# Optimization experiments

Hardware: AMD Instinct MI355X
Metric: run time of the kernel (lower is better)

The kernel has to match this reference:

```python
import jax, jax.numpy as jnp
import numpy as np


def setup_inputs() -> dict:
    key = jax.random.key(0)
    k1, k2, k3, k4 = jax.random.split(key, 4)
    B, T, L, C, F = 1024, 128, 256, 2, 784
    x = jax.random.normal(k1, (B, T, F), dtype=jnp.float32)
    W = jax.random.normal(k2, (L, F), dtype=jnp.float32) * (1.0 / np.sqrt(F))
    b = jax.random.normal(k3, (L,), dtype=jnp.float32) * 0.01
    contribution = jax.random.normal(k4, (T, L, C), dtype=jnp.float32)
    return {"x": x, "W": W, "b": b, "contribution": contribution}


def reference(x, W, b, contribution):
    # symbolic_paths: Linear(784 -> leaf) + Hardtanh  -> [B, T, L]
    sp = jnp.clip(jnp.einsum('btf,lf->btl', x, W) + b, -1.0, 1.0)
    # per-(tree,leaf) outer product: class_value[b,t,l,c] = sp[b,t,l] * contribution[t,l,c]
    cv = sp[..., None] * contribution[None]          # [B, T, L, C]
    p = jax.nn.softmax(cv, axis=-1)                  # softmax over classes
    gini = jnp.sum(1.0 - p * p, axis=-1)             # [B, T, L]
    return (sp, gini)
```

## Files before the change

### kernel.cpp

```cpp
#include <hip/hip_runtime.h>
#include <hip/hip_bf16.h>

typedef __attribute__((ext_vector_type(8))) short bf16x8;
typedef __attribute__((ext_vector_type(4))) float f32x4;

#define B_SZ   1024
#define T_SZ   128
#define L_SZ   256
#define F_SZ   784
#define M_TOT  (B_SZ * T_SZ)
#define BK     32
#define KSTEPS 25
#define KCHUNKS 100
#define BROWS  32

#define WPRE_ELEMS (KSTEPS * 4 * L_SZ)
#define WPRE_BYTES (WPRE_ELEMS * 16)
#define CDIFF_ELEMS (T_SZ * L_SZ)
#define WS_NEED (WPRE_BYTES + CDIFF_ELEMS * 4)

__device__ __forceinline__ unsigned short f2bf(float f) {
    __hip_bfloat16 h = __float2bfloat16(f);
    return *reinterpret_cast<unsigned short*>(&h);
}

__global__ __launch_bounds__(256) void dn_prep(
    const float* __restrict__ W, const float* __restrict__ contrib,
    unsigned short* __restrict__ wpre, float* __restrict__ cdiff)
{
    const int gid = blockIdx.x * 256 + threadIdx.x;
    if (gid < WPRE_ELEMS) {
        const int leaf = gid & 255;
        const int kg   = (gid >> 8) & 3;
        const int ks   = gid >> 10;
        const int k0   = ks * BK + kg * 8;
        bf16x8 v;
        #pragma unroll
        for (int j = 0; j < 8; ++j) {
            const int k = k0 + j;
            const float f = (k < F_SZ) ? W[(size_t)leaf * F_SZ + k] : 0.f;
            v[j] = (short)f2bf(f);
        }
        *reinterpret_cast<bf16x8*>(wpre + (size_t)gid * 8) = v;
    } else {
        const int cid = gid - WPRE_ELEMS;
        if (cid < CDIFF_ELEMS)
            cdiff[cid] = contrib[(size_t)cid * 2] - contrib[(size_t)cid * 2 + 1];
    }
}

__global__ __launch_bounds__(512, 6) void dn_fused7(
    const float* __restrict__ x, const unsigned short* __restrict__ wpre,
    const float* __restrict__ bias, const float* __restrict__ cdiff,
    float* __restrict__ out)
{
    __shared__ __align__(16) unsigned char smem[KCHUNKS * BROWS * 16];
    bf16x8* As = reinterpret_cast<bf16x8*>(smem);
    typedef float OtRow[264];
    OtRow* Ot = reinterpret_cast<OtRow*>(smem);

    const int tid  = threadIdx.x;
    const int lane = tid & 63;
    const int wid  = tid >> 6;
    const int lr   = lane & 15;
    const int kseg = lane >> 4;

    const int rowBase = blockIdx.x * BROWS;
    const int colBase = wid * 32;

    #pragma unroll
    for (int it = 0; it < 7; ++it) {
        const int i = it * 512 + tid;
        if (i < BROWS * KCHUNKS) {
            const int row = i / KCHUNKS;
            const int kc  = i - row * KCHUNKS;
            bf16x8 v;
            if (kc < 98) {
                const float* p = x + (size_t)(rowBase + row) * F_SZ + kc * 8;
                const f32x4 lo = *reinterpret_cast<const f32x4*>(p);
                const f32x4 hi = *reinterpret_cast<const f32x4*>(p + 4);
                #pragma unroll
                for (int j = 0; j < 4; ++j) {
                    v[j]     = (short)f2bf(lo[j]);
                    v[4 + j] = (short)f2bf(hi[j]);
                }
            } else {
                #pragma unroll
                for (int j = 0; j < 8; ++j) v[j] = 0;
            }
            As[kc * BROWS + (row ^ (kc & 7))] = v;
        }
    }
    __syncthreads();

    const unsigned short* wpb = wpre + ((size_t)kseg * L_SZ + colBase + lr) * 8;

    f32x4 acc[2][2];
    #pragma unroll
    for (int mi = 0; mi < 2; ++mi)
        #pragma unroll
        for (int ni = 0; ni < 2; ++ni)
            acc[mi][ni] = (f32x4){0.f, 0.f, 0.f, 0.f};

    bf16x8 wcur[2], wnxt[2];
    wcur[0] = *reinterpret_cast<const bf16x8*>(wpb);
    wcur[1] = *reinterpret_cast<const bf16x8*>(wpb + 128);

    #pragma unroll
    for (int ks = 0; ks < KSTEPS; ++ks) {
        if (ks + 1 < KSTEPS) {
            wnxt[0] = *reinterpret_cast<const bf16x8*>(wpb + (size_t)(ks + 1) * 8192);
            wnxt[1] = *reinterpret_cast<const bf16x8*>(wpb + (size_t)(ks + 1) * 8192 + 128);
        }
        const int kcr = ks * 4 + kseg;
        const bf16x8 a0 = As[kcr * BROWS + (lr ^ (kcr & 7))];
        const bf16x8 a1 = As[kcr * BROWS + ((16 + lr) ^ (kcr & 7))];

        acc[0][0] = __builtin_amdgcn_mfma_f32_16x16x32_bf16(a0, wcur[0], acc[0][0], 0, 0, 0);
        acc[0][1] = __builtin_amdgcn_mfma_f32_16x16x32_bf16(a0, wcur[1], acc[0][1], 0, 0, 0);
        acc[1][0] = __builtin_amdgcn_mfma_f32_16x16x32_bf16(a1, wcur[0], acc[1][0], 0, 0, 0);
        acc[1][1] = __builtin_amdgcn_mfma_f32_16x16x32_bf16(a1, wcur[1], acc[1][1], 0, 0, 0);

        wcur[0] = wnxt[0];
        wcur[1] = wnxt[1];
    }
    __syncthreads();

    float spv[2][2][4];
    #pragma unroll
    for (int ni = 0; ni < 2; ++ni) {
        const float bb = bias[colBase + ni * 16 + lr];
        #pragma unroll
        for (int mi = 0; mi < 2; ++mi)
            #pragma unroll
            for (int r = 0; r < 4; ++r)
                spv[mi][ni][r] = fminf(fmaxf(acc[mi][ni][r] + bb, -1.f), 1.f);
    }

    const int erow = tid >> 4;
    const int ecol = (tid & 15) * 4;
    const size_t GOFF = (size_t)M_TOT * L_SZ;
    float* orow = out + (size_t)(rowBase + erow) * L_SZ;

    #pragma unroll
    for (int ni = 0; ni < 2; ++ni)
        #pragma unroll
        for (int mi = 0; mi < 2; ++mi)
            #pragma unroll
            for (int r = 0; r < 4; ++r)
                Ot[mi * 16 + kseg * 4 + r][colBase + ni * 16 + lr] = spv[mi][ni][r];
    __syncthreads();
    #pragma unroll
    for (int j = 0; j < 4; ++j) {
        const f32x4 v = *reinterpret_cast<const f32x4*>(&Ot[erow][ecol + 64 * j]);
        *reinterpret_cast<f32x4*>(orow + ecol + 64 * j) = v;
    }
    __syncthreads();

    #pragma unroll
    for (int ni = 0; ni < 2; ++ni) {
        const int col = colBase + ni * 16 + lr;
        #pragma unroll
        for (int mi = 0; mi < 2; ++mi)
            #pragma unroll
            for (int r = 0; r < 4; ++r) {
                const int t = (rowBase + mi * 16 + kseg * 4 + r) & (T_SZ - 1);
                const float d  = spv[mi][ni][r] * cdiff[t * L_SZ + col];
                const float ed = __expf(d);
                const float s2 = ed / (1.f + ed);
                Ot[mi * 16 + kseg * 4 + r][col] = fmaf(2.f * s2, 1.f - s2, 1.f);
            }
    }
    __syncthreads();
    #pragma unroll
    for (int j = 0; j < 4; ++j) {
        const f32x4 v = *reinterpret_cast<const f32x4*>(&Ot[erow][ecol + 64 * j]);
        *reinterpret_cast<f32x4*>(orow + GOFF + ecol + 64 * j) = v;
    }
}

__global__ __launch_bounds__(512) void dn_fused_v1(
    const float* __restrict__ x, const float* __restrict__ W,
    const float* __restrict__ bias, const float* __restrict__ contrib,
    float* __restrict__ out)
{
    __shared__ bf16x8 As[4][128];
    __shared__ bf16x8 Bs[4][L_SZ];

    const int tid    = threadIdx.x;
    const int lane   = tid & 63;
    const int wid    = tid >> 6;
    const int waveM  = wid >> 2;
    const int waveN  = wid & 3;
    const int blkRow = blockIdx.x * 128;
    const int ar = tid >> 2;
    const int ak = (tid & 3) * 8;
    const int wr = tid >> 1;
    const int wk = (tid & 1) * 16;
    const int laneRow = lane & 15;
    const int kgrp    = lane >> 4;

    f32x4 acc[4][4];
    #pragma unroll
    for (int i = 0; i < 4; ++i)
        #pragma unroll
        for (int j = 0; j < 4; ++j)
            acc[i][j] = (f32x4){0.f, 0.f, 0.f, 0.f};

    const float* xrow = x + (size_t)(blkRow + ar) * F_SZ;
    const float* wrow = W + (size_t)wr * F_SZ;
    const f32x4 zf = {0.f, 0.f, 0.f, 0.f};

    f32x4 xa0 = *reinterpret_cast<const f32x4*>(xrow + ak);
    f32x4 xa1 = *reinterpret_cast<const f32x4*>(xrow + ak + 4);
    f32x4 wa0 = *reinterpret_cast<const f32x4*>(wrow + wk);
    f32x4 wa1 = *reinterpret_cast<const f32x4*>(wrow + wk + 4);
    f32x4 wa2 = *reinterpret_cast<const f32x4*>(wrow + wk + 8);
    f32x4 wa3 = *reinterpret_cast<const f32x4*>(wrow + wk + 12);

    for (int ks = 0; ks < KSTEPS; ++ks) {
        bf16x8 av, wv0, wv1;
        #pragma unroll
        for (int j = 0; j < 4; ++j) {
            av[j]      = (short)f2bf(xa0[j]);
            av[4 + j]  = (short)f2bf(xa1[j]);
            wv0[j]     = (short)f2bf(wa0[j]);
            wv0[4 + j] = (short)f2bf(wa1[j]);
            wv1[j]     = (short)f2bf(wa2[j]);
            wv1[4 + j] = (short)f2bf(wa3[j]);
        }
        As[ak >> 3][ar] = av;
        Bs[wk >> 3][wr] = wv0;
        Bs[(wk >> 3) + 1][wr] = wv1;
        __syncthreads();

        if (ks + 1 < KSTEPS) {
            const int kb = (ks + 1) * BK;
            if (kb + ak < F_SZ) {
                xa0 = *reinterpret_cast<const f32x4*>(xrow + kb + ak);
                xa1 = *reinterpret_cast<const f32x4*>(xrow + kb + ak + 4);
            } else { xa0 = zf; xa1 = zf; }
            if (kb + wk < F_SZ) {
                wa0 = *reinterpret_cast<const f32x4*>(wrow + kb + wk);
                wa1 = *reinterpret_cast<const f32x4*>(wrow + kb + wk + 4);
                wa2 = *reinterpret_cast<const f32x4*>(wrow + kb + wk + 8);
                wa3 = *reinterpret_cast<const f32x4*>(wrow + kb + wk + 12);
            } else { wa0 = zf; wa1 = zf; wa2 = zf; wa3 = zf; }
        }

        bf16x8 af[4], bfv[4];
        #pragma unroll
        for (int mi = 0; mi < 4; ++mi)
            af[mi] = As[kgrp][waveM * 64 + mi * 16 + laneRow];
        #pragma unroll
        for (int ni = 0; ni < 4; ++ni)
            bfv[ni] = Bs[kgrp][waveN * 64 + ni * 16 + laneRow];
        #pragma unroll
        for (int mi = 0; mi < 4; ++mi)
            #pragma unroll
            for (int ni = 0; ni < 4; ++ni)
                acc[mi][ni] = __builtin_amdgcn_mfma_f32_16x16x32_bf16(
                    af[mi], bfv[ni], acc[mi][ni], 0, 0, 0);
        __syncthreads();
    }

    const size_t GOFF  = (size_t)M_TOT * L_SZ;
    const int    rbase = waveM * 64 + (lane >> 4) * 4;
    const int    cbase = waveN * 64 + laneRow;
    #pragma unroll
    for (int ni = 0; ni < 4; ++ni) {
        const int col = cbase + ni * 16;
        const float bb = bias[col];
        #pragma unroll
        for (int mi = 0; mi < 4; ++mi) {
            #pragma unroll
            for (int r = 0; r < 4; ++r) {
                const int m = blkRow + rbase + mi * 16 + r;
                const int t = m & (T_SZ - 1);
                float v  = acc[mi][ni][r] + bb;
                float sp = fminf(fmaxf(v, -1.f), 1.f);
                const float* cp = contrib + (size_t)(t * L_SZ + col) * 2;
                const float d  = sp * (cp[0] - cp[1]);
                const float ed = __expf(d);
                const float s  = ed / (1.f + ed);
                const float g  = fmaf(2.f * s, 1.f - s, 1.f);
                const size_t o = (size_t)m * L_SZ + col;
                out[o]        = sp;
                out[GOFF + o] = g;
            }
        }
    }
}

extern "C" void kernel_launch(void* const* d_in, const int* in_sizes, int n_in,
                              void* d_out, int out_size, void* d_ws, size_t ws_size,
                              hipStream_t stream) {
    const float* x       = (const float*)d_in[0];
    const float* W       = (const float*)d_in[1];
    const float* bias    = (const float*)d_in[2];
    const float* contrib = (const float*)d_in[3];
    float* out = (float*)d_out;

    if (ws_size >= (size_t)WS_NEED && d_ws != nullptr) {
        unsigned short* wpre  = (unsigned short*)d_ws;
        float*          cdiff = (float*)((char*)d_ws + WPRE_BYTES);
        const int prep_threads = WPRE_ELEMS + CDIFF_ELEMS;
        dn_prep<<<(prep_threads + 255) / 256, 256, 0, stream>>>(W, contrib, wpre, cdiff);
        dn_fused7<<<M_TOT / BROWS, 512, 0, stream>>>(x, wpre, bias, cdiff, out);
    } else {
        dn_fused_v1<<<M_TOT / 128, 512, 0, stream>>>(x, W, bias, contrib, out);
    }
}
```

Before: 186.5 us.

## Pipeline x tile loads into LDS chunk-by-chunk overlapping MFMA compute

Instead of staging the whole 32x784 x tile into LDS before any MFMA work, the kernel loads the first 16 k-chunks, then in each of 7 phases prefetches the next 16 chunks into registers while computing on the already resident chunks, converts and stores them afterward, and synchronises per phase. This hides global-load latency behind matrix compute within a block. Launch bounds drop from 6 to 3 blocks per CU's worth of waves, allowing more registers for the in-flight prefetch but possibly reducing occupancy, and the added per-phase barriers cost some synchronisation.

```diff
diff --git a/kernel.cpp b/kernel.cpp
--- a/kernel.cpp
+++ b/kernel.cpp
@@ -49,7 +49,7 @@
     }
 }
 
-__global__ __launch_bounds__(512, 6) void dn_fused7(
+__global__ __launch_bounds__(512, 3) void dn_fused9(
     const float* __restrict__ x, const unsigned short* __restrict__ wpre,
     const float* __restrict__ bias, const float* __restrict__ cdiff,
     float* __restrict__ out)
@@ -68,28 +68,29 @@
     const int rowBase = blockIdx.x * BROWS;
     const int colBase = wid * 32;
 
-    #pragma unroll
-    for (int it = 0; it < 7; ++it) {
-        const int i = it * 512 + tid;
-        if (i < BROWS * KCHUNKS) {
-            const int row = i / KCHUNKS;
-            const int kc  = i - row * KCHUNKS;
-            bf16x8 v;
-            if (kc < 98) {
-                const float* p = x + (size_t)(rowBase + row) * F_SZ + kc * 8;
-                const f32x4 lo = *reinterpret_cast<const f32x4*>(p);
-                const f32x4 hi = *reinterpret_cast<const f32x4*>(p + 4);
-                #pragma unroll
-                for (int j = 0; j < 4; ++j) {
-                    v[j]     = (short)f2bf(lo[j]);
-                    v[4 + j] = (short)f2bf(hi[j]);
-                }
-            } else {
-                #pragma unroll
-                for (int j = 0; j < 8; ++j) v[j] = 0;
-            }
-            As[kc * BROWS + (row ^ (kc & 7))] = v;
-        }
+    const int srow = tid >> 4;
+    const int skc  = tid & 15;
+    const float* sbase = x + (size_t)(rowBase + srow) * F_SZ;
+    const int trow = tid >> 1;
+    const int tkc  = 96 + (tid & 1);
+
+    f32x4 slo, shi;
+
+    if (tid < 64) {
+        const int zr = tid >> 1, zk = 98 + (tid & 1);
+        bf16x8 z;
+        #pragma unroll
+        for (int j = 0; j < 8; ++j) z[j] = 0;
+        As[zk * BROWS + (zr ^ (zk & 7))] = z;
+    }
+    {
+        const float* p0 = sbase + skc * 8;
+        slo = *reinterpret_cast<const f32x4*>(p0);
+        shi = *reinterpret_cast<const f32x4*>(p0 + 4);
+        bf16x8 v;
+        #pragma unroll
+        for (int j = 0; j < 4; ++j) { v[j] = (short)f2bf(slo[j]); v[4+j] = (short)f2bf(shi[j]); }
+        As[skc * BROWS + (srow ^ (skc & 7))] = v;
     }
     __syncthreads();
 
@@ -107,24 +108,55 @@
     wcur[1] = *reinterpret_cast<const bf16x8*>(wpb + 128);
 
     #pragma unroll
-    for (int ks = 0; ks < KSTEPS; ++ks) {
-        if (ks + 1 < KSTEPS) {
-            wnxt[0] = *reinterpret_cast<const bf16x8*>(wpb + (size_t)(ks + 1) * 8192);
-            wnxt[1] = *reinterpret_cast<const bf16x8*>(wpb + (size_t)(ks + 1) * 8192 + 128);
-        }
-        const int kcr = ks * 4 + kseg;
-        const bf16x8 a0 = As[kcr * BROWS + (lr ^ (kcr & 7))];
-        const bf16x8 a1 = As[kcr * BROWS + ((16 + lr) ^ (kcr & 7))];
-
-        acc[0][0] = __builtin_amdgcn_mfma_f32_16x16x32_bf16(a0, wcur[0], acc[0][0], 0, 0, 0);
-        acc[0][1] = __builtin_amdgcn_mfma_f32_16x16x32_bf16(a0, wcur[1], acc[0][1], 0, 0, 0);
-        acc[1][0] = __builtin_amdgcn_mfma_f32_16x16x32_bf16(a1, wcur[0], acc[1][0], 0, 0, 0);
-        acc[1][1] = __builtin_amdgcn_mfma_f32_16x16x32_bf16(a1, wcur[1], acc[1][1], 0, 0, 0);
-
-        wcur[0] = wnxt[0];
-        wcur[1] = wnxt[1];
-    }
-    __syncthreads();
+    for (int p = 0; p < 7; ++p) {
+        if (p < 5) {
+            const float* pn = sbase + (16 * (p + 1) + skc) * 8;
+            slo = *reinterpret_cast<const f32x4*>(pn);
+            shi = *reinterpret_cast<const f32x4*>(pn + 4);
+        } else if (p == 5) {
+            if (tid < 64) {
+                const float* pn = x + (size_t)(rowBase + trow) * F_SZ + tkc * 8;
+                slo = *reinterpret_cast<const f32x4*>(pn);
+                shi = *reinterpret_cast<const f32x4*>(pn + 4);
+            }
+        }
+
+        const int ks0 = 4 * p;
+        const int ks1 = (p < 6) ? 4 * p + 4 : 25;
+        #pragma unroll
+        for (int ks = ks0; ks < ks1; ++ks) {
+            if (ks + 1 < KSTEPS) {
+                wnxt[0] = *reinterpret_cast<const bf16x8*>(wpb + (size_t)(ks + 1) * 8192);
+                wnxt[1] = *reinterpret_cast<const bf16x8*>(wpb + (size_t)(ks + 1) * 8192 + 128);
+            }
+            const int kcr = ks * 4 + kseg;
+            const bf16x8 a0 = As[kcr * BROWS + (lr ^ (kcr & 7))];
+            const bf16x8 a1 = As[kcr * BROWS + ((16 + lr) ^ (kcr & 7))];
+
+            acc[0][0] = __builtin_amdgcn_mfma_f32_16x16x32_bf16(a0, wcur[0], acc[0][0], 0, 0, 0);
+            acc[0][1] = __builtin_amdgcn_mfma_f32_16x16x32_bf16(a0, wcur[1], acc[0][1], 0, 0, 0);
+            acc[1][0] = __builtin_amdgcn_mfma_f32_16x16x32_bf16(a1, wcur[0], acc[1][0], 0, 0, 0);
+            acc[1][1] = __builtin_amdgcn_mfma_f32_16x16x32_bf16(a1, wcur[1], acc[1][1], 0, 0, 0);
+            wcur[0] = wnxt[0];
+            wcur[1] = wnxt[1];
+        }
+
+        if (p < 5) {
+            const int kc = 16 * (p + 1) + skc;
+            bf16x8 v;
+            #pragma unroll
+            for (int j = 0; j < 4; ++j) { v[j] = (short)f2bf(slo[j]); v[4+j] = (short)f2bf(shi[j]); }
+            As[kc * BROWS + (srow ^ (kc & 7))] = v;
+        } else if (p == 5) {
+            if (tid < 64) {
+                bf16x8 v;
+                #pragma unroll
+                for (int j = 0; j < 4; ++j) { v[j] = (short)f2bf(slo[j]); v[4+j] = (short)f2bf(shi[j]); }
+                As[tkc * BROWS + (trow ^ (tkc & 7))] = v;
+            }
+        }
+        __syncthreads();
+    }
 
     float spv[2][2][4];
     #pragma unroll
@@ -306,7 +338,7 @@
         float*          cdiff = (float*)((char*)d_ws + WPRE_BYTES);
         const int prep_threads = WPRE_ELEMS + CDIFF_ELEMS;
         dn_prep<<<(prep_threads + 255) / 256, 256, 0, stream>>>(W, contrib, wpre, cdiff);
-        dn_fused7<<<M_TOT / BROWS, 512, 0, stream>>>(x, wpre, bias, cdiff, out);
+        dn_fused9<<<M_TOT / BROWS, 512, 0, stream>>>(x, wpre, bias, cdiff, out);
     } else {
         dn_fused_v1<<<M_TOT / 128, 512, 0, stream>>>(x, W, bias, contrib, out);
     }
```

Result: slower. 191.7 us (+2.8%).

## Rewrite fused GEMM with 128-row tiles and double-buffered global_load_lds pipeline

Applied to the files above, without the earlier changes.

Replaces the 32-row-per-block kernel with a 128-row tile in which each wave computes a 64x64 sub-tile. The x and W k-slices go straight from global memory into a double-buffered, swizzled LDS buffer via global_load_lds, with s_waitcnt and barriers so the next step loads while the current step runs MFMAs. x is now staged as fp32 and converted to bf16 when read from LDS, and the epilogue writes sp and gini in four 32-row chunks. The larger tile is meant to cut repeated W traffic and to hide load latency, at the cost of more registers, 64KB of LDS and lower occupancy.

```diff
diff --git a/kernel.cpp b/kernel.cpp
--- a/kernel.cpp
+++ b/kernel.cpp
@@ -11,8 +11,6 @@
 #define M_TOT  (B_SZ * T_SZ)
 #define BK     32
 #define KSTEPS 25
-#define KCHUNKS 100
-#define BROWS  32
 
 #define WPRE_ELEMS (KSTEPS * 4 * L_SZ)
 #define WPRE_BYTES (WPRE_ELEMS * 16)
@@ -49,133 +47,188 @@
     }
 }
 
-__global__ __launch_bounds__(512, 6) void dn_fused7(
+
+#define GLDS(g, l)                                                           \
+    __builtin_amdgcn_global_load_lds(                                        \
+        (const __attribute__((address_space(1))) void*)(g),                  \
+        (__attribute__((address_space(3))) void*)(l), 16, 0, 0)
+
+__global__ __launch_bounds__(512, 4) void dn_fused11(
     const float* __restrict__ x, const unsigned short* __restrict__ wpre,
     const float* __restrict__ bias, const float* __restrict__ cdiff,
     float* __restrict__ out)
 {
-    __shared__ __align__(16) unsigned char smem[KCHUNKS * BROWS * 16];
-    bf16x8* As = reinterpret_cast<bf16x8*>(smem);
+    __shared__ __align__(16) unsigned char smem[65536];
+
+    const int tid   = threadIdx.x;
+    const int lane  = tid & 63;
+    const int wid   = tid >> 6;
+    const int lr    = lane & 15;
+    const int kseg  = lane >> 4;
+    const int waveM = wid >> 2;
+    const int wN    = wid & 3;
+
+    const int rowBase = blockIdx.x * 128;
+
+    const int s0  = wid * 2048 + lane * 16;
+    const int s1  = s0 + 1024;
+    const int r0  = s0 >> 7, r1 = s1 >> 7;
+    const int og0 = (s0 & 127) ^ ((r0 & 7) << 4);
+    const int og1 = (s1 & 127) ^ ((r1 & 7) << 4);
+
+    const char* xA0 = (const char*)x + (size_t)(rowBase + r0) * 3136 + og0;
+    const char* xA1 = (const char*)x + (size_t)(rowBase + r1) * 3136 + og1;
+    const char* xA0t = (const char*)x + (size_t)(rowBase + r0) * 3136
+                       + (og0 < 64 ? 3072 + og0 : 0);
+    const char* xA1t = (const char*)x + (size_t)(rowBase + r1) * 3136
+                       + (og1 < 64 ? 3072 + og1 : 0);
+
+    const int wg0 = s0 ^ (((s0 >> 12) & 3) << 4);
+    const int wg1 = s1 ^ (((s1 >> 12) & 3) << 4);
+    const char* wS0 = (const char*)wpre + wg0;
+    const char* wS1 = (const char*)wpre + wg1;
+
+    const int ldsA0 = wid * 2048;
+    const int ldsA1 = ldsA0 + 1024;
+    const int ldsW0 = 32768 + wid * 2048;
+    const int ldsW1 = ldsW0 + 1024;
+
+    #define ISSUE_STEP(k) do {                                               \
+        const int _b = ((k) & 1) * 16384;                                    \
+        if ((k) < 24) {                                                      \
+            GLDS(xA0 + (size_t)(k) * 128, smem + _b + ldsA0);                \
+            GLDS(xA1 + (size_t)(k) * 128, smem + _b + ldsA1);                \
+        } else {                                                             \
+            GLDS(xA0t, smem + _b + ldsA0);                                   \
+            GLDS(xA1t, smem + _b + ldsA1);                                   \
+        }                                                                    \
+        GLDS(wS0 + (size_t)(k) * 16384, smem + _b + ldsW0);                  \
+        GLDS(wS1 + (size_t)(k) * 16384, smem + _b + ldsW1);                  \
+    } while (0)
+
+    f32x4 acc[4][4];
+    #pragma unroll
+    for (int mi = 0; mi < 4; ++mi)
+        #pragma unroll
+        for (int ni = 0; ni < 4; ++ni)
+            acc[mi][ni] = (f32x4){0.f, 0.f, 0.f, 0.f};
+
+    ISSUE_STEP(0);
+    asm volatile("s_waitcnt vmcnt(0)" ::: "memory");
+    __builtin_amdgcn_s_barrier();
+
+    #pragma unroll
+    for (int k = 0; k < KSTEPS; ++k) {
+        if (k + 1 < KSTEPS) {
+            ISSUE_STEP(k + 1);
+            asm volatile("s_waitcnt vmcnt(4)" ::: "memory");
+        } else {
+            asm volatile("s_waitcnt vmcnt(0)" ::: "memory");
+        }
+        __builtin_amdgcn_s_barrier();
+
+        const unsigned char* Ab = smem + (k & 1) * 16384;
+        const unsigned char* Wb = Ab + 32768;
+
+        bf16x8 wf[4];
+        #pragma unroll
+        for (int ni = 0; ni < 4; ++ni) {
+            const int Lw = kseg * 4096 + (wN * 64 + ni * 16 + lr) * 16;
+            wf[ni] = *reinterpret_cast<const bf16x8*>(Wb + (Lw ^ (kseg << 4)));
+        }
+        #pragma unroll
+        for (int mi = 0; mi < 4; ++mi) {
+            const int row = waveM * 64 + mi * 16 + lr;
+            const int sw  = (row & 7) << 4;
+            const f32x4 alo = *reinterpret_cast<const f32x4*>(
+                Ab + row * 128 + ((kseg * 32) ^ sw));
+            const f32x4 ahi = *reinterpret_cast<const f32x4*>(
+                Ab + row * 128 + ((kseg * 32 + 16) ^ sw));
+            bf16x8 af;
+            #pragma unroll
+            for (int j = 0; j < 4; ++j) {
+                af[j]     = (short)f2bf(alo[j]);
+                af[4 + j] = (short)f2bf(ahi[j]);
+            }
+            #pragma unroll
+            for (int ni = 0; ni < 4; ++ni)
+                acc[mi][ni] = __builtin_amdgcn_mfma_f32_16x16x32_bf16(
+                    af, wf[ni], acc[mi][ni], 0, 0, 0);
+        }
+        __builtin_amdgcn_s_barrier();
+    }
+    #undef ISSUE_STEP
+
+    float spv[4][4][4];
+    #pragma unroll
+    for (int ni = 0; ni < 4; ++ni) {
+        const float bb = bias[wN * 64 + ni * 16 + lr];
+        #pragma unroll
+        for (int mi = 0; mi < 4; ++mi)
+            #pragma unroll
+            for (int r = 0; r < 4; ++r)
+                spv[mi][ni][r] = fminf(fmaxf(acc[mi][ni][r] + bb, -1.f), 1.f);
+    }
+
     typedef float OtRow[264];
     OtRow* Ot = reinterpret_cast<OtRow*>(smem);
 
-    const int tid  = threadIdx.x;
-    const int lane = tid & 63;
-    const int wid  = tid >> 6;
-    const int lr   = lane & 15;
-    const int kseg = lane >> 4;
-
-    const int rowBase = blockIdx.x * BROWS;
-    const int colBase = wid * 32;
-
-    #pragma unroll
-    for (int it = 0; it < 7; ++it) {
-        const int i = it * 512 + tid;
-        if (i < BROWS * KCHUNKS) {
-            const int row = i / KCHUNKS;
-            const int kc  = i - row * KCHUNKS;
-            bf16x8 v;
-            if (kc < 98) {
-                const float* p = x + (size_t)(rowBase + row) * F_SZ + kc * 8;
-                const f32x4 lo = *reinterpret_cast<const f32x4*>(p);
-                const f32x4 hi = *reinterpret_cast<const f32x4*>(p + 4);
+    const int erow = tid >> 4;
+    const int ecol = (tid & 15) * 16;
+    const size_t GOFF = (size_t)M_TOT * L_SZ;
+
+    __syncthreads();
+
+    #pragma unroll
+    for (int q = 0; q < 4; ++q) {
+        const int qrow = rowBase + q * 32;
+        if (waveM == (q >> 1)) {
+            #pragma unroll
+            for (int m2 = 0; m2 < 2; ++m2) {
+                const int mi = (q & 1) * 2 + m2;
                 #pragma unroll
-                for (int j = 0; j < 4; ++j) {
-                    v[j]     = (short)f2bf(lo[j]);
-                    v[4 + j] = (short)f2bf(hi[j]);
+                for (int ni = 0; ni < 4; ++ni)
+                    #pragma unroll
+                    for (int r = 0; r < 4; ++r)
+                        Ot[m2 * 16 + kseg * 4 + r][wN * 64 + ni * 16 + lr]
+                            = spv[mi][ni][r];
+            }
+        }
+        __syncthreads();
+        #pragma unroll
+        for (int j = 0; j < 4; ++j) {
+            const f32x4 v = *reinterpret_cast<const f32x4*>(&Ot[erow][ecol + j * 4]);
+            *reinterpret_cast<f32x4*>(out + (size_t)(qrow + erow) * L_SZ
+                                      + ecol + j * 4) = v;
+        }
+        __syncthreads();
+        if (waveM == (q >> 1)) {
+            #pragma unroll
+            for (int m2 = 0; m2 < 2; ++m2) {
+                const int mi = (q & 1) * 2 + m2;
+                #pragma unroll
+                for (int ni = 0; ni < 4; ++ni) {
+                    const int col = wN * 64 + ni * 16 + lr;
+                    #pragma unroll
+                    for (int r = 0; r < 4; ++r) {
+                        const int t = q * 32 + m2 * 16 + kseg * 4 + r;
+                        const float d  = spv[mi][ni][r] * cdiff[t * L_SZ + col];
+                        const float ed = __expf(d);
+                        const float s2 = ed / (1.f + ed);
+                        Ot[m2 * 16 + kseg * 4 + r][col]
+                            = fmaf(2.f * s2, 1.f - s2, 1.f);
+                    }
                 }
-            } else {
-                #pragma unroll
-                for (int j = 0; j < 8; ++j) v[j] = 0;
             }
-            As[kc * BROWS + (row ^ (kc & 7))] = v;
-        }
-    }
-    __syncthreads();
-
-    const unsigned short* wpb = wpre + ((size_t)kseg * L_SZ + colBase + lr) * 8;
-
-    f32x4 acc[2][2];
-    #pragma unroll
-    for (int mi = 0; mi < 2; ++mi)
-        #pragma unroll
-        for (int ni = 0; ni < 2; ++ni)
-            acc[mi][ni] = (f32x4){0.f, 0.f, 0.f, 0.f};
-
-    bf16x8 wcur[2], wnxt[2];
-    wcur[0] = *reinterpret_cast<const bf16x8*>(wpb);
-    wcur[1] = *reinterpret_cast<const bf16x8*>(wpb + 128);
-
-    #pragma unroll
-    for (int ks = 0; ks < KSTEPS; ++ks) {
-        if (ks + 1 < KSTEPS) {
-            wnxt[0] = *reinterpret_cast<const bf16x8*>(wpb + (size_t)(ks + 1) * 8192);
-            wnxt[1] = *reinterpret_cast<const bf16x8*>(wpb + (size_t)(ks + 1) * 8192 + 128);
-        }
-        const int kcr = ks * 4 + kseg;
-        const bf16x8 a0 = As[kcr * BROWS + (lr ^ (kcr & 7))];
-        const bf16x8 a1 = As[kcr * BROWS + ((16 + lr) ^ (kcr & 7))];
-
-        acc[0][0] = __builtin_amdgcn_mfma_f32_16x16x32_bf16(a0, wcur[0], acc[0][0], 0, 0, 0);
-        acc[0][1] = __builtin_amdgcn_mfma_f32_16x16x32_bf16(a0, wcur[1], acc[0][1], 0, 0, 0);
-        acc[1][0] = __builtin_amdgcn_mfma_f32_16x16x32_bf16(a1, wcur[0], acc[1][0], 0, 0, 0);
-        acc[1][1] = __builtin_amdgcn_mfma_f32_16x16x32_bf16(a1, wcur[1], acc[1][1], 0, 0, 0);
-
-        wcur[0] = wnxt[0];
-        wcur[1] = wnxt[1];
-    }
-    __syncthreads();
-
-    float spv[2][2][4];
-    #pragma unroll
-    for (int ni = 0; ni < 2; ++ni) {
-        const float bb = bias[colBase + ni * 16 + lr];
-        #pragma unroll
-        for (int mi = 0; mi < 2; ++mi)
-            #pragma unroll
-            for (int r = 0; r < 4; ++r)
-                spv[mi][ni][r] = fminf(fmaxf(acc[mi][ni][r] + bb, -1.f), 1.f);
-    }
-
-    const int erow = tid >> 4;
-    const int ecol = (tid & 15) * 4;
-    const size_t GOFF = (size_t)M_TOT * L_SZ;
-    float* orow = out + (size_t)(rowBase + erow) * L_SZ;
-
-    #pragma unroll
-    for (int ni = 0; ni < 2; ++ni)
-        #pragma unroll
-        for (int mi = 0; mi < 2; ++mi)
-            #pragma unroll
-            for (int r = 0; r < 4; ++r)
-                Ot[mi * 16 + kseg * 4 + r][colBase + ni * 16 + lr] = spv[mi][ni][r];
-    __syncthreads();
-    #pragma unroll
-    for (int j = 0; j < 4; ++j) {
-        const f32x4 v = *reinterpret_cast<const f32x4*>(&Ot[erow][ecol + 64 * j]);
-        *reinterpret_cast<f32x4*>(orow + ecol + 64 * j) = v;
-    }
-    __syncthreads();
-
-    #pragma unroll
-    for (int ni = 0; ni < 2; ++ni) {
-        const int col = colBase + ni * 16 + lr;
-        #pragma unroll
-        for (int mi = 0; mi < 2; ++mi)
-            #pragma unroll
-            for (int r = 0; r < 4; ++r) {
-                const int t = (rowBase + mi * 16 + kseg * 4 + r) & (T_SZ - 1);
-                const float d  = spv[mi][ni][r] * cdiff[t * L_SZ + col];
-                const float ed = __expf(d);
-                const float s2 = ed / (1.f + ed);
-                Ot[mi * 16 + kseg * 4 + r][col] = fmaf(2.f * s2, 1.f - s2, 1.f);
-            }
-    }
-    __syncthreads();
-    #pragma unroll
-    for (int j = 0; j < 4; ++j) {
-        const f32x4 v = *reinterpret_cast<const f32x4*>(&Ot[erow][ecol + 64 * j]);
-        *reinterpret_cast<f32x4*>(orow + GOFF + ecol + 64 * j) = v;
+        }
+        __syncthreads();
+        #pragma unroll
+        for (int j = 0; j < 4; ++j) {
+            const f32x4 v = *reinterpret_cast<const f32x4*>(&Ot[erow][ecol + j * 4]);
+            *reinterpret_cast<f32x4*>(out + GOFF + (size_t)(qrow + erow) * L_SZ
+                                      + ecol + j * 4) = v;
+        }
+        __syncthreads();
     }
 }
 
@@ -306,7 +359,7 @@
         float*          cdiff = (float*)((char*)d_ws + WPRE_BYTES);
         const int prep_threads = WPRE_ELEMS + CDIFF_ELEMS;
         dn_prep<<<(prep_threads + 255) / 256, 256, 0, stream>>>(W, contrib, wpre, cdiff);
-        dn_fused7<<<M_TOT / BROWS, 512, 0, stream>>>(x, wpre, bias, cdiff, out);
+        dn_fused11<<<M_TOT / 128, 512, 0, stream>>>(x, wpre, bias, cdiff, out);
     } else {
         dn_fused_v1<<<M_TOT / 128, 512, 0, stream>>>(x, W, bias, contrib, out);
     }
```

Result: slower. 219.4 us (+17.7%).

## Double-buffer fp32 x tiles via direct global-to-LDS loads overlapping MFMA

Applied to the files above, without the earlier changes.

Replaces the single up-front load of the 32-row x tile, which converted to bf16 before LDS, with a five-window double-buffered pipeline. Each window is fetched as raw fp32 using global_load_lds directly into shared memory while the previous window is consumed. The bf16 conversion now happens after the LDS read, inside the MFMA loop. This is meant to hide global latency behind compute, at the cost of twice the LDS traffic per element, extra conversion work in the inner loop, and per-window waitcnt and barrier synchronisation.

```diff
diff --git a/kernel.cpp b/kernel.cpp
--- a/kernel.cpp
+++ b/kernel.cpp
@@ -11,13 +11,15 @@
 #define M_TOT  (B_SZ * T_SZ)
 #define BK     32
 #define KSTEPS 25
-#define KCHUNKS 100
-#define BROWS  32
 
 #define WPRE_ELEMS (KSTEPS * 4 * L_SZ)
 #define WPRE_BYTES (WPRE_ELEMS * 16)
 #define CDIFF_ELEMS (T_SZ * L_SZ)
 #define WS_NEED (WPRE_BYTES + CDIFF_ELEMS * 4)
+
+#define ROWB   656
+#define WINB   (32 * ROWB)
+#define BUFB   21504
 
 __device__ __forceinline__ unsigned short f2bf(float f) {
     __hip_bfloat16 h = __float2bfloat16(f);
@@ -49,15 +51,18 @@
     }
 }
 
-__global__ __launch_bounds__(512, 6) void dn_fused7(
+
+#define GLDS(g, l)                                                           \
+    __builtin_amdgcn_global_load_lds(                                        \
+        (const __attribute__((address_space(1))) void*)(g),                  \
+        (__attribute__((address_space(3))) void*)(l), 16, 0, 0)
+
+__global__ __launch_bounds__(512, 6) void dn_fused12(
     const float* __restrict__ x, const unsigned short* __restrict__ wpre,
     const float* __restrict__ bias, const float* __restrict__ cdiff,
     float* __restrict__ out)
 {
-    __shared__ __align__(16) unsigned char smem[KCHUNKS * BROWS * 16];
-    bf16x8* As = reinterpret_cast<bf16x8*>(smem);
-    typedef float OtRow[264];
-    OtRow* Ot = reinterpret_cast<OtRow*>(smem);
+    __shared__ __align__(16) unsigned char smem[2 * BUFB];
 
     const int tid  = threadIdx.x;
     const int lane = tid & 63;
@@ -65,35 +70,37 @@
     const int lr   = lane & 15;
     const int kseg = lane >> 4;
 
-    const int rowBase = blockIdx.x * BROWS;
+    const int rowBase = blockIdx.x * 32;
     const int colBase = wid * 32;
 
-    #pragma unroll
-    for (int it = 0; it < 7; ++it) {
-        const int i = it * 512 + tid;
-        if (i < BROWS * KCHUNKS) {
-            const int row = i / KCHUNKS;
-            const int kc  = i - row * KCHUNKS;
-            bf16x8 v;
-            if (kc < 98) {
-                const float* p = x + (size_t)(rowBase + row) * F_SZ + kc * 8;
-                const f32x4 lo = *reinterpret_cast<const f32x4*>(p);
-                const f32x4 hi = *reinterpret_cast<const f32x4*>(p + 4);
-                #pragma unroll
-                for (int j = 0; j < 4; ++j) {
-                    v[j]     = (short)f2bf(lo[j]);
-                    v[4 + j] = (short)f2bf(hi[j]);
-                }
-            } else {
-                #pragma unroll
-                for (int j = 0; j < 8; ++j) v[j] = 0;
-            }
-            As[kc * BROWS + (row ^ (kc & 7))] = v;
-        }
-    }
-    __syncthreads();
-
-    const unsigned short* wpb = wpre + ((size_t)kseg * L_SZ + colBase + lr) * 8;
+    const char* xb = (const char*)x;
+    const char* srcB[3];
+    const char* srcC[3];
+    bool        v4[3];
+    #pragma unroll
+    for (int jj = 0; jj < 3; ++jj) {
+        const int j = wid + 8 * jj;
+        const unsigned s    = j * 1024 + lane * 16;
+        const unsigned row  = s / ROWB;
+        const unsigned colb = s - row * ROWB;
+        const bool     ok   = (row < 32) && (colb < 640);
+        const unsigned rcl  = (row < 32) ? row : 0;
+        srcC[jj] = xb + (size_t)(rowBase + rcl) * 3136;
+        srcB[jj] = srcC[jj] + (ok ? colb : 0);
+        v4[jj]   = ok && (colb < 576);
+    }
+
+    #define ISSUE(w) do {                                                    \
+        _Pragma("unroll")                                                    \
+        for (int _jj = 0; _jj < 3; ++_jj) {                                  \
+            const int _j = wid + 8 * _jj;                                    \
+            if (_j < 21) {                                                   \
+                const char* _s = ((w) < 4) ? (srcB[_jj] + (w) * 640)         \
+                                : (v4[_jj] ? srcB[_jj] + 2560 : srcC[_jj]);  \
+                GLDS(_s, smem + ((w) & 1) * BUFB + _j * 1024);               \
+            }                                                                \
+        }                                                                    \
+    } while (0)
 
     f32x4 acc[2][2];
     #pragma unroll
@@ -102,29 +109,51 @@
         for (int ni = 0; ni < 2; ++ni)
             acc[mi][ni] = (f32x4){0.f, 0.f, 0.f, 0.f};
 
+    const unsigned short* wpb = wpre + ((size_t)kseg * L_SZ + colBase + lr) * 8;
     bf16x8 wcur[2], wnxt[2];
+
+    ISSUE(0);
     wcur[0] = *reinterpret_cast<const bf16x8*>(wpb);
     wcur[1] = *reinterpret_cast<const bf16x8*>(wpb + 128);
-
-    #pragma unroll
-    for (int ks = 0; ks < KSTEPS; ++ks) {
-        if (ks + 1 < KSTEPS) {
-            wnxt[0] = *reinterpret_cast<const bf16x8*>(wpb + (size_t)(ks + 1) * 8192);
-            wnxt[1] = *reinterpret_cast<const bf16x8*>(wpb + (size_t)(ks + 1) * 8192 + 128);
-        }
-        const int kcr = ks * 4 + kseg;
-        const bf16x8 a0 = As[kcr * BROWS + (lr ^ (kcr & 7))];
-        const bf16x8 a1 = As[kcr * BROWS + ((16 + lr) ^ (kcr & 7))];
-
-        acc[0][0] = __builtin_amdgcn_mfma_f32_16x16x32_bf16(a0, wcur[0], acc[0][0], 0, 0, 0);
-        acc[0][1] = __builtin_amdgcn_mfma_f32_16x16x32_bf16(a0, wcur[1], acc[0][1], 0, 0, 0);
-        acc[1][0] = __builtin_amdgcn_mfma_f32_16x16x32_bf16(a1, wcur[0], acc[1][0], 0, 0, 0);
-        acc[1][1] = __builtin_amdgcn_mfma_f32_16x16x32_bf16(a1, wcur[1], acc[1][1], 0, 0, 0);
-
-        wcur[0] = wnxt[0];
-        wcur[1] = wnxt[1];
-    }
-    __syncthreads();
+    asm volatile("s_waitcnt vmcnt(0)" ::: "memory");
+    __builtin_amdgcn_s_barrier();
+
+    #pragma unroll
+    for (int w = 0; w < 5; ++w) {
+        if (w < 4) ISSUE(w + 1);
+
+        const unsigned char* Ab = smem + (w & 1) * BUFB;
+        #pragma unroll
+        for (int i = 0; i < 5; ++i) {
+            const int ks = w * 5 + i;
+            if (ks + 1 < KSTEPS) {
+                wnxt[0] = *reinterpret_cast<const bf16x8*>(wpb + (size_t)(ks + 1) * 8192);
+                wnxt[1] = *reinterpret_cast<const bf16x8*>(wpb + (size_t)(ks + 1) * 8192 + 128);
+            }
+            bf16x8 af[2];
+            #pragma unroll
+            for (int m = 0; m < 2; ++m) {
+                const int off = (m * 16 + lr) * ROWB + i * 128 + kseg * 32;
+                const f32x4 alo = *reinterpret_cast<const f32x4*>(Ab + off);
+                const f32x4 ahi = *reinterpret_cast<const f32x4*>(Ab + off + 16);
+                #pragma unroll
+                for (int jd = 0; jd < 4; ++jd) {
+                    af[m][jd]     = (short)f2bf(alo[jd]);
+                    af[m][4 + jd] = (short)f2bf(ahi[jd]);
+                }
+            }
+            acc[0][0] = __builtin_amdgcn_mfma_f32_16x16x32_bf16(af[0], wcur[0], acc[0][0], 0, 0, 0);
+            acc[0][1] = __builtin_amdgcn_mfma_f32_16x16x32_bf16(af[0], wcur[1], acc[0][1], 0, 0, 0);
+            acc[1][0] = __builtin_amdgcn_mfma_f32_16x16x32_bf16(af[1], wcur[0], acc[1][0], 0, 0, 0);
+            acc[1][1] = __builtin_amdgcn_mfma_f32_16x16x32_bf16(af[1], wcur[1], acc[1][1], 0, 0, 0);
+            wcur[0] = wnxt[0];
+            wcur[1] = wnxt[1];
+        }
+        asm volatile("s_waitcnt vmcnt(0)" ::: "memory");
+        __builtin_amdgcn_sched_barrier(0);
+        __builtin_amdgcn_s_barrier();
+    }
+    #undef ISSUE
 
     float spv[2][2][4];
     #pragma unroll
@@ -136,6 +165,9 @@
             for (int r = 0; r < 4; ++r)
                 spv[mi][ni][r] = fminf(fmaxf(acc[mi][ni][r] + bb, -1.f), 1.f);
     }
+
+    typedef float OtRow[264];
+    OtRow* Ot = reinterpret_cast<OtRow*>(smem);
 
     const int erow = tid >> 4;
     const int ecol = (tid & 15) * 4;
@@ -306,7 +338,7 @@
         float*          cdiff = (float*)((char*)d_ws + WPRE_BYTES);
         const int prep_threads = WPRE_ELEMS + CDIFF_ELEMS;
         dn_prep<<<(prep_threads + 255) / 256, 256, 0, stream>>>(W, contrib, wpre, cdiff);
-        dn_fused7<<<M_TOT / BROWS, 512, 0, stream>>>(x, wpre, bias, cdiff, out);
+        dn_fused12<<<M_TOT / 32, 512, 0, stream>>>(x, wpre, bias, cdiff, out);
     } else {
         dn_fused_v1<<<M_TOT / 128, 512, 0, stream>>>(x, W, bias, contrib, out);
     }
```

Measured after the change: 190.0 us. About the same (+1.9%).
